# Optimization experiments

Hardware: AMD Instinct MI355X
Metric: run time of the kernel (lower is better)

## Reference

```python
import jax, jax.numpy as jnp
import numpy as np

N_NODES = 100000
N_EDGES = 1600000
IN_SIZE = 512
HID_SIZE = 256
OUT_SIZE = 40
K_STEPS = 10
ALPHA = 0.1


def setup_inputs() -> dict:
    key = jax.random.key(0)
    ks = jax.random.split(key, 8)
    features = jax.random.normal(ks[0], (N_NODES, IN_SIZE), dtype=jnp.float32)
    src = jax.random.randint(ks[1], (N_EDGES,), 0, N_NODES, dtype=jnp.int64)
    dst = jax.random.randint(ks[2], (N_EDGES,), 0, N_NODES, dtype=jnp.int64)
    # MLP params (Kaiming-ish scale)
    W1 = jax.random.normal(ks[3], (IN_SIZE, HID_SIZE), dtype=jnp.float32) / np.sqrt(IN_SIZE)
    b1 = jnp.zeros((HID_SIZE,), dtype=jnp.float32)
    W2 = jax.random.normal(ks[4], (HID_SIZE, OUT_SIZE), dtype=jnp.float32) / np.sqrt(HID_SIZE)
    b2 = jnp.zeros((OUT_SIZE,), dtype=jnp.float32)
    return {"features": features, "src": src, "dst": dst,
            "W1": W1, "b1": b1, "W2": W2, "b2": b2}


def reference(features, src, dst, W1, b1, W2, b2):
    # --- MLP encoder (dropout is identity in eval mode) ---
    h = jax.nn.relu(features @ W1 + b1)
    h = h @ W2 + b2  # [N, out_size]

    # --- Symmetric normalization (DGL APPNPConv, edge_weight=None) ---
    ones_e = jnp.ones((src.shape[0],), dtype=h.dtype)
    deg_out = jax.ops.segment_sum(ones_e, src, num_segments=N_NODES)
    deg_in = jax.ops.segment_sum(ones_e, dst, num_segments=N_NODES)
    norm_src = jnp.power(jnp.clip(deg_out, 1.0), -0.5)[:, None]  # D_out^{-1/2}
    norm_dst = jnp.power(jnp.clip(deg_in, 1.0), -0.5)[:, None]   # D_in^{-1/2}

    # --- k=10 APPNP propagation: h <- (1-a) * D^{-1/2} A D^{-1/2} h + a * h0 ---
    h0 = h

    def step(h, _):
        msg = (h * norm_src)[src]                                  # gather [E, out]
        agg = jax.ops.segment_sum(msg, dst, num_segments=N_NODES)  # scatter-add
        h = (1.0 - ALPHA) * (agg * norm_dst) + ALPHA * h0
        return h, None

    h, _ = jax.lax.scan(step, h, None, length=K_STEPS)
    return h
```

## Files before the change

### kernel.cpp

```cpp
#include <hip/hip_runtime.h>

#define N_NODES 100000
#define N_EDGES 1600000
#define IN_SIZE 512
#define HID_SIZE 256
#define OUT_SIZE 40
#define K_STEPS 10
#define ALPHA 0.1f

#define NCH 250
#define CH_E 6400
#define NBUK 391
#define NRS 8
#define HRS 12544
#define NCS 16
#define CS_E 100000

typedef _Float16 half8 __attribute__((ext_vector_type(8)));
typedef float f32x4 __attribute__((ext_vector_type(4)));

struct __align__(8) Entry { int s; int d; };

__global__ __launch_bounds__(512) void hist_pass(const int* __restrict__ dst,
                                                 int* __restrict__ cnt) {
    __shared__ int h[NBUK];
    const int t = threadIdx.x, c = blockIdx.x;
    for (int j = t; j < NBUK; j += 512) h[j] = 0;
    __syncthreads();
    const int4* d4 = (const int4*)(dst + c * CH_E);
    for (int i = t; i < CH_E / 4; i += 512) {
        const int4 v = d4[i];
        atomicAdd(&h[v.x >> 8], 1);
        atomicAdd(&h[v.y >> 8], 1);
        atomicAdd(&h[v.z >> 8], 1);
        atomicAdd(&h[v.w >> 8], 1);
    }
    __syncthreads();
    for (int j = t; j < NBUK; j += 512) cnt[c * NBUK + j] = h[j];
}

__global__ __launch_bounds__(512) void bucket_scan(const int* __restrict__ cnt,
                                                   int* __restrict__ off,
                                                   int* __restrict__ boff) {
    __shared__ int tot[512];
    const int b = threadIdx.x;
    int s = 0;
    if (b < NBUK)
        for (int c = 0; c < NCH; ++c) s += cnt[c * NBUK + b];
    tot[b] = s;
    __syncthreads();
    for (int o = 1; o < 512; o <<= 1) {
        const int v = (b >= o) ? tot[b - o] : 0;
        __syncthreads();
        tot[b] += v;
        __syncthreads();
    }
    if (b < NBUK) {
        int run = tot[b] - s;
        boff[b] = run;
        for (int c = 0; c < NCH; ++c) { off[c * NBUK + b] = run; run += cnt[c * NBUK + b]; }
        if (b == NBUK - 1) boff[NBUK] = tot[b];
    }
}

__global__ __launch_bounds__(512) void scatter_pass(const int* __restrict__ src,
                                                    const int* __restrict__ dst,
                                                    const int* __restrict__ off,
                                                    Entry* __restrict__ ebuf) {
    __shared__ int cur[NBUK];
    const int t = threadIdx.x, c = blockIdx.x;
    for (int j = t; j < NBUK; j += 512) cur[j] = off[c * NBUK + j];
    __syncthreads();
    const int4* s4 = (const int4*)(src + c * CH_E);
    const int4* d4 = (const int4*)(dst + c * CH_E);
    for (int i = t; i < CH_E / 4; i += 512) {
        const int4 sv = s4[i];
        const int4 dv = d4[i];
        Entry e;
        int p;
        p = atomicAdd(&cur[dv.x >> 8], 1); e.s = sv.x; e.d = dv.x; ebuf[p] = e;
        p = atomicAdd(&cur[dv.y >> 8], 1); e.s = sv.y; e.d = dv.y; ebuf[p] = e;
        p = atomicAdd(&cur[dv.z >> 8], 1); e.s = sv.z; e.d = dv.z; ebuf[p] = e;
        p = atomicAdd(&cur[dv.w >> 8], 1); e.s = sv.w; e.d = dv.w; ebuf[p] = e;
    }
}

__global__ __launch_bounds__(256) void bucket_csr(const Entry* __restrict__ ebuf,
                                                  const int* __restrict__ boff,
                                                  int* __restrict__ rowp,
                                                  float* __restrict__ ndst,
                                                  int* __restrict__ csr) {
    __shared__ int hist[256];
    __shared__ int pref[256];
    __shared__ int cur[256];
    const int t = threadIdx.x, b = blockIdx.x;
    const int beg = boff[b], end = boff[b + 1];
    hist[t] = 0;
    __syncthreads();
    for (int i = beg + t; i < end; i += 256)
        atomicAdd(&hist[ebuf[i].d & 255], 1);
    __syncthreads();
    const int h = hist[t];
    pref[t] = h;
    __syncthreads();
    for (int o = 1; o < 256; o <<= 1) {
        const int v = (t >= o) ? pref[t - o] : 0;
        __syncthreads();
        pref[t] += v;
        __syncthreads();
    }
    const int val = beg + pref[t] - h;
    const int n = (b << 8) + t;
    if (n <= N_NODES) rowp[n] = val;
    if (n < N_NODES) ndst[n] = 1.0f / sqrtf((float)max(h, 1));
    cur[t] = val;
    __syncthreads();
    for (int i = beg + t; i < end; i += 256) {
        const Entry e = ebuf[i];
        const int pos = atomicAdd(&cur[e.d & 255], 1);
        csr[pos] = e.s;
    }
}

__global__ __launch_bounds__(512) void degsrc_part(const int* __restrict__ src,
                                                   int* __restrict__ partial) {
    __shared__ int h[HRS];
    const int t = threadIdx.x;
    const int r = blockIdx.x & (NRS - 1);
    const int c = blockIdx.x >> 3;
    const int base = r * HRS;
    for (int j = t; j < HRS; j += 512) h[j] = 0;
    __syncthreads();
    const int4* s4 = (const int4*)(src + (size_t)c * CS_E);
    for (int i = t; i < CS_E / 4; i += 512) {
        const int4 v = s4[i];
        unsigned u;
        u = (unsigned)(v.x - base); if (u < HRS) atomicAdd(&h[u], 1);
        u = (unsigned)(v.y - base); if (u < HRS) atomicAdd(&h[u], 1);
        u = (unsigned)(v.z - base); if (u < HRS) atomicAdd(&h[u], 1);
        u = (unsigned)(v.w - base); if (u < HRS) atomicAdd(&h[u], 1);
    }
    __syncthreads();
    for (int j = t; j < HRS; j += 512) partial[(size_t)c * (NRS * HRS) + base + j] = h[j];
}

__global__ __launch_bounds__(256) void nsrc_reduce(const int* __restrict__ partial,
                                                   float* __restrict__ nsrc) {
    const int n = blockIdx.x * 256 + threadIdx.x;
    int s = 0;
#pragma unroll
    for (int c = 0; c < NCS; ++c) s += partial[(size_t)c * (NRS * HRS) + n];
    if (n < N_NODES) nsrc[n] = 1.0f / sqrtf((float)max(s, 1));
}

__global__ __launch_bounds__(256) void prep_w1t(const float* __restrict__ W1,
                                                unsigned short* __restrict__ w1t) {
    int idx = blockIdx.x * 256 + threadIdx.x;
    if (idx < IN_SIZE * HID_SIZE) {
        int n = idx >> 9;
        int k = idx & 511;
        _Float16 h = (_Float16)W1[(size_t)k * HID_SIZE + n];
        w1t[idx] = *(unsigned short*)&h;
    }
}

__global__ __launch_bounds__(512) void gemm1_f16(const float* __restrict__ X,
                                                 const unsigned short* __restrict__ w1t,
                                                 const float* __restrict__ b1,
                                                 _Float16* __restrict__ h1) {
    __shared__ __align__(16) _Float16 sA[128 * 64];
    __shared__ __align__(16) _Float16 sB[256 * 64];

    const int t    = threadIdx.x;
    const int lane = t & 63;
    const int w    = t >> 6;
    const int wr   = w >> 2;
    const int wc   = w & 3;
    const int n0   = blockIdx.x * 128;

    f32x4 acc[4][4];
#pragma unroll
    for (int i = 0; i < 4; ++i)
#pragma unroll
        for (int j = 0; j < 4; ++j) acc[i][j] = (f32x4)0.f;

    const int lo = lane & 15;
    const int hi = lane >> 4;
    const int l7 = lane & 7;

    for (int kk = 0; kk < IN_SIZE; kk += 64) {
        __syncthreads();
#pragma unroll
        for (int i = 0; i < 2; ++i) {
            int id  = t + i * 512;
            int row = id >> 3;
            int ch  = id & 7;
            int gr  = n0 + row;
            float4 x0 = make_float4(0.f, 0.f, 0.f, 0.f), x1 = x0;
            if (gr < N_NODES) {
                const float* p = X + (size_t)gr * IN_SIZE + kk + ch * 8;
                x0 = ((const float4*)p)[0];
                x1 = ((const float4*)p)[1];
            }
            half8 hv;
            hv[0] = (_Float16)x0.x; hv[1] = (_Float16)x0.y;
            hv[2] = (_Float16)x0.z; hv[3] = (_Float16)x0.w;
            hv[4] = (_Float16)x1.x; hv[5] = (_Float16)x1.y;
            hv[6] = (_Float16)x1.z; hv[7] = (_Float16)x1.w;
            *(half8*)&sA[row * 64 + ((ch ^ (row & 7)) << 3)] = hv;
        }
#pragma unroll
        for (int i = 0; i < 4; ++i) {
            int id = t + i * 512;
            int n  = id >> 3;
            int ch = id & 7;
            uint4 v = *(const uint4*)(w1t + (size_t)n * IN_SIZE + kk + ch * 8);
            *(uint4*)&sB[n * 64 + ((ch ^ (n & 7)) << 3)] = v;
        }
        __syncthreads();
#pragma unroll
        for (int s = 0; s < 2; ++s) {
            const int chs = ((s * 4 + hi) ^ l7) << 3;
            half8 af[4], bf[4];
#pragma unroll
            for (int f = 0; f < 4; ++f)
                af[f] = *(const half8*)&sA[(wr * 64 + f * 16 + lo) * 64 + chs];
#pragma unroll
            for (int f = 0; f < 4; ++f)
                bf[f] = *(const half8*)&sB[(wc * 64 + f * 16 + lo) * 64 + chs];
#pragma unroll
            for (int fi = 0; fi < 4; ++fi)
#pragma unroll
                for (int fj = 0; fj < 4; ++fj)
                    acc[fi][fj] = __builtin_amdgcn_mfma_f32_16x16x32_f16(
                        af[fi], bf[fj], acc[fi][fj], 0, 0, 0);
        }
    }

    float b1v[4];
#pragma unroll
    for (int fj = 0; fj < 4; ++fj) b1v[fj] = b1[wc * 64 + fj * 16 + lo];
#pragma unroll
    for (int fi = 0; fi < 4; ++fi) {
#pragma unroll
        for (int fj = 0; fj < 4; ++fj) {
            const int col = wc * 64 + fj * 16 + lo;
#pragma unroll
            for (int r = 0; r < 4; ++r) {
                int grow = n0 + wr * 64 + fi * 16 + hi * 4 + r;
                if (grow < N_NODES) {
                    float v = acc[fi][fj][r] + b1v[fj];
                    v = fmaxf(v, 0.f);
                    h1[(size_t)grow * HID_SIZE + col] = (_Float16)v;
                }
            }
        }
    }
}

__global__ __launch_bounds__(256) void gemm2(const _Float16* __restrict__ h1,
                                             const float* __restrict__ W2,
                                             const float* __restrict__ b2,
                                             float* __restrict__ h0) {
    __shared__ __align__(16) float sW2t[40 * 260];
    __shared__ __align__(16) unsigned short sH[64 * 264];

    const int t  = threadIdx.x;
    const int n0 = blockIdx.x * 64;

    for (int idx = t; idx < HID_SIZE * OUT_SIZE; idx += 256) {
        int c = idx / OUT_SIZE;
        int o = idx - c * OUT_SIZE;
        sW2t[o * 260 + c] = W2[idx];
    }
#pragma unroll
    for (int i = 0; i < 8; ++i) {
        int id  = t + i * 256;
        int row = id >> 5;
        int ch  = id & 31;
        uint4 v = make_uint4(0, 0, 0, 0);
        if (n0 + row < N_NODES)
            v = *(const uint4*)(h1 + (size_t)(n0 + row) * HID_SIZE + ch * 8);
        *(uint4*)&sH[row * 264 + ch * 8] = v;
    }
    __syncthreads();

    const int r2 = t >> 2;
    const int q  = t & 3;
    const int o0 = q * 10;
    float acc2[10];
#pragma unroll
    for (int m = 0; m < 10; ++m) acc2[m] = b2[o0 + m];

    for (int c = 0; c < HID_SIZE; c += 8) {
        uint4 hv = *(const uint4*)&sH[r2 * 264 + c];
        const _Float16* hp = (const _Float16*)&hv;
        float f[8];
#pragma unroll
        for (int j = 0; j < 8; ++j) f[j] = (float)hp[j];
#pragma unroll
        for (int m = 0; m < 10; ++m) {
            const float4 w0 = *(const float4*)&sW2t[(o0 + m) * 260 + c];
            const float4 w1 = *(const float4*)&sW2t[(o0 + m) * 260 + c + 4];
            acc2[m] += f[0] * w0.x + f[1] * w0.y + f[2] * w0.z + f[3] * w0.w
                     + f[4] * w1.x + f[5] * w1.y + f[6] * w1.z + f[7] * w1.w;
        }
    }
    if (n0 + r2 < N_NODES) {
        float* dstp = h0 + (size_t)(n0 + r2) * OUT_SIZE + o0;
#pragma unroll
        for (int m = 0; m < 10; ++m) dstp[m] = acc2[m];
    }
}

__global__ __launch_bounds__(320) void g0_init(const float* __restrict__ h0,
                                               const float* __restrict__ nsrc,
                                               _Float16* __restrict__ g) {
    const int tid = threadIdx.x;
    const int ln  = tid / 5;
    const int q   = tid - ln * 5;
    const int n   = blockIdx.x * 64 + ln;
    if (n >= N_NODES) return;
    const float ns = nsrc[n];
    const f32x4 a = *(const f32x4*)(h0 + (size_t)n * OUT_SIZE + q * 8);
    const f32x4 b = *(const f32x4*)(h0 + (size_t)n * OUT_SIZE + q * 8 + 4);
    half8 gv;
    gv[0] = (_Float16)(ns * a[0]); gv[1] = (_Float16)(ns * a[1]);
    gv[2] = (_Float16)(ns * a[2]); gv[3] = (_Float16)(ns * a[3]);
    gv[4] = (_Float16)(ns * b[0]); gv[5] = (_Float16)(ns * b[1]);
    gv[6] = (_Float16)(ns * b[2]); gv[7] = (_Float16)(ns * b[3]);
    *(half8*)(g + (size_t)n * 64 + q * 8) = gv;
}

__global__ __launch_bounds__(320) void appnp_step3(const _Float16* __restrict__ gin,
                                                   const float* __restrict__ h0,
                                                   const int* __restrict__ rowp,
                                                   const int* __restrict__ csr,
                                                   const float* __restrict__ nsrc,
                                                   const float* __restrict__ ndst,
                                                   _Float16* __restrict__ gout,
                                                   float* __restrict__ hout,
                                                   int last) {
    const int tid = threadIdx.x;
    const int ln  = tid / 5;
    const int q   = tid - ln * 5;
    const int n   = blockIdx.x * 64 + ln;
    if (n >= N_NODES) return;

    const int beg = rowp[n];
    const int end = rowp[n + 1];
    const _Float16* gq = gin + q * 8;

    float acc[8];
#pragma unroll
    for (int j = 0; j < 8; ++j) acc[j] = 0.f;

    int e = beg;
    for (; e + 4 <= end; e += 4) {
        const int s0 = csr[e + 0];
        const int s1 = csr[e + 1];
        const int s2 = csr[e + 2];
        const int s3 = csr[e + 3];
        const half8 v0 = *(const half8*)(gq + (size_t)s0 * 64);
        const half8 v1 = *(const half8*)(gq + (size_t)s1 * 64);
        const half8 v2 = *(const half8*)(gq + (size_t)s2 * 64);
        const half8 v3 = *(const half8*)(gq + (size_t)s3 * 64);
#pragma unroll
        for (int j = 0; j < 8; ++j)
            acc[j] += (float)v0[j] + (float)v1[j] + (float)v2[j] + (float)v3[j];
    }
    for (; e < end; ++e) {
        const int s0 = csr[e];
        const half8 v0 = *(const half8*)(gq + (size_t)s0 * 64);
#pragma unroll
        for (int j = 0; j < 8; ++j) acc[j] += (float)v0[j];
    }

    const float nd = (1.0f - ALPHA) * ndst[n];
    const f32x4 h0a = *(const f32x4*)(h0 + (size_t)n * OUT_SIZE + q * 8);
    const f32x4 h0b = *(const f32x4*)(h0 + (size_t)n * OUT_SIZE + q * 8 + 4);
    float r[8];
    r[0] = nd * acc[0] + ALPHA * h0a[0]; r[1] = nd * acc[1] + ALPHA * h0a[1];
    r[2] = nd * acc[2] + ALPHA * h0a[2]; r[3] = nd * acc[3] + ALPHA * h0a[3];
    r[4] = nd * acc[4] + ALPHA * h0b[0]; r[5] = nd * acc[5] + ALPHA * h0b[1];
    r[6] = nd * acc[6] + ALPHA * h0b[2]; r[7] = nd * acc[7] + ALPHA * h0b[3];

    if (last) {
        f32x4 ra, rb;
        ra[0] = r[0]; ra[1] = r[1]; ra[2] = r[2]; ra[3] = r[3];
        rb[0] = r[4]; rb[1] = r[5]; rb[2] = r[6]; rb[3] = r[7];
        *(f32x4*)(hout + (size_t)n * OUT_SIZE + q * 8) = ra;
        *(f32x4*)(hout + (size_t)n * OUT_SIZE + q * 8 + 4) = rb;
    } else {
        const float ns = nsrc[n];
        half8 gv;
#pragma unroll
        for (int j = 0; j < 8; ++j) gv[j] = (_Float16)(ns * r[j]);
        *(half8*)(gout + (size_t)n * 64 + q * 8) = gv;
    }
}

extern "C" void kernel_launch(void* const* d_in, const int* in_sizes, int n_in,
                              void* d_out, int out_size, void* d_ws, size_t ws_size,
                              hipStream_t stream) {
    const float* X   = (const float*)d_in[0];
    const int*   src = (const int*)d_in[1];
    const int*   dst = (const int*)d_in[2];
    const float* W1  = (const float*)d_in[3];
    const float* b1  = (const float*)d_in[4];
    const float* W2  = (const float*)d_in[5];
    const float* b2  = (const float*)d_in[6];
    float* out = (float*)d_out;

    char* ws = (char*)d_ws;
    size_t off = 0;
    auto alloc = [&](size_t bytes) -> void* {
        void* p = ws + off;
        off = (off + bytes + 255) & ~(size_t)255;
        return p;
    };
    float* h0 = (float*)alloc((size_t)N_NODES * OUT_SIZE * 4);
    const size_t mark = off;

    unsigned short* w1t = (unsigned short*)alloc((size_t)IN_SIZE * HID_SIZE * 2);
    _Float16*       h1  = (_Float16*)alloc((size_t)N_NODES * HID_SIZE * 2);

    off = mark;
    _Float16* gA = (_Float16*)alloc((size_t)N_NODES * 64 * 2);
    _Float16* gB = (_Float16*)alloc((size_t)N_NODES * 64 * 2);
    int*   partial = (int*)gA;
    Entry* ebuf    = (Entry*)gB;
    float* nsrc = (float*)alloc((size_t)N_NODES * 4);
    float* ndst = (float*)alloc((size_t)N_NODES * 4);
    int* rowp   = (int*)alloc((size_t)(N_NODES + 2) * 4);
    int* csr    = (int*)alloc((size_t)N_EDGES * 4);
    int* cnt    = (int*)alloc((size_t)NCH * NBUK * 4);
    int* offb   = (int*)alloc((size_t)NCH * NBUK * 4);
    int* boff   = (int*)alloc((size_t)(NBUK + 1) * 4);

    const int pgrid = (N_NODES + 63) / 64;

    prep_w1t<<<(IN_SIZE * HID_SIZE + 255) / 256, 256, 0, stream>>>(W1, w1t);
    gemm1_f16<<<(N_NODES + 127) / 128, 512, 0, stream>>>(X, w1t, b1, h1);
    gemm2<<<(N_NODES + 63) / 64, 256, 0, stream>>>(h1, W2, b2, h0);

    hist_pass<<<NCH, 512, 0, stream>>>(dst, cnt);
    bucket_scan<<<1, 512, 0, stream>>>(cnt, offb, boff);
    scatter_pass<<<NCH, 512, 0, stream>>>(src, dst, offb, ebuf);
    bucket_csr<<<NBUK, 256, 0, stream>>>(ebuf, boff, rowp, ndst, csr);

    degsrc_part<<<NRS * NCS, 512, 0, stream>>>(src, partial);
    nsrc_reduce<<<(NRS * HRS) / 256, 256, 0, stream>>>(partial, nsrc);

    g0_init<<<pgrid, 320, 0, stream>>>(h0, nsrc, gA);

    const _Float16* gin = gA;
    for (int s = 0; s < K_STEPS; ++s) {
        const int last = (s == K_STEPS - 1) ? 1 : 0;
        _Float16* gout = (s & 1) ? gA : gB;
        appnp_step3<<<pgrid, 320, 0, stream>>>(gin, h0, rowp, csr, nsrc, ndst,
                                               gout, out, last);
        gin = gout;
    }
}
```

Baseline: 550.2 us.

## Fuse MLP layers and g0 init into one MFMA kernel with fp16 h0

Merges the first GEMM, the second GEMM (now on MFMA with a padded fp16 W2^T) and the g0 initialisation into a single kernel. The hidden activations stay in LDS instead of making a round trip through a global h1 buffer. The GEMM1 main loop also register-prefetches the next K-slice of X and W1 so loads overlap compute. The residual term is stored once as fp16 ALPHA*h0 in 64-wide rows, which removes the fp32 h0 reads in every propagation step at some cost in precision.

```diff
diff --git a/kernel.cpp b/kernel.cpp
--- a/kernel.cpp
+++ b/kernel.cpp
@@ -153,23 +153,39 @@
     if (n < N_NODES) nsrc[n] = 1.0f / sqrtf((float)max(s, 1));
 }
 
-__global__ __launch_bounds__(256) void prep_w1t(const float* __restrict__ W1,
-                                                unsigned short* __restrict__ w1t) {
+__global__ __launch_bounds__(256) void prep_w(const float* __restrict__ W1,
+                                              const float* __restrict__ W2,
+                                              unsigned short* __restrict__ w1t,
+                                              unsigned short* __restrict__ w2t) {
     int idx = blockIdx.x * 256 + threadIdx.x;
     if (idx < IN_SIZE * HID_SIZE) {
         int n = idx >> 9;
         int k = idx & 511;
         _Float16 h = (_Float16)W1[(size_t)k * HID_SIZE + n];
         w1t[idx] = *(unsigned short*)&h;
-    }
-}
-
-__global__ __launch_bounds__(512) void gemm1_f16(const float* __restrict__ X,
-                                                 const unsigned short* __restrict__ w1t,
-                                                 const float* __restrict__ b1,
-                                                 _Float16* __restrict__ h1) {
-    __shared__ __align__(16) _Float16 sA[128 * 64];
-    __shared__ __align__(16) _Float16 sB[256 * 64];
+    } else if (idx < IN_SIZE * HID_SIZE + 48 * HID_SIZE) {
+        int i2 = idx - IN_SIZE * HID_SIZE;
+        int o = i2 >> 8;
+        int c = i2 & 255;
+        float v = (o < OUT_SIZE) ? W2[(size_t)c * OUT_SIZE + o] : 0.f;
+        _Float16 h = (_Float16)v;
+        w2t[i2] = *(unsigned short*)&h;
+    }
+}
+
+__global__ __launch_bounds__(512) void gemm_fused(const float* __restrict__ X,
+                                                  const unsigned short* __restrict__ w1t,
+                                                  const float* __restrict__ b1,
+                                                  const unsigned short* __restrict__ w2t,
+                                                  const float* __restrict__ b2,
+                                                  const float* __restrict__ nsrc,
+                                                  _Float16* __restrict__ h0a,
+                                                  _Float16* __restrict__ g0) {
+    __shared__ __align__(16) unsigned char lds[49152];
+    _Float16* sA = (_Float16*)lds;
+    _Float16* sB = sA + 128 * 64;
+    _Float16* sC = (_Float16*)lds;
+    _Float16* sW = sC + 128 * 72;
 
     const int t    = threadIdx.x;
     const int lane = t & 63;
@@ -188,34 +204,61 @@
     const int hi = lane >> 4;
     const int l7 = lane & 7;
 
+    int rowA[2], offA[2]; bool okA[2]; const float* pA[2];
+#pragma unroll
+    for (int i = 0; i < 2; ++i) {
+        const int id  = t + i * 512;
+        const int row = id >> 3;
+        const int ch  = id & 7;
+        rowA[i] = row;
+        offA[i] = row * 64 + ((ch ^ (row & 7)) << 3);
+        const int gr = n0 + row;
+        okA[i] = (gr < N_NODES);
+        pA[i] = X + (size_t)(okA[i] ? gr : 0) * IN_SIZE + ch * 8;
+    }
+    int offB[4]; const unsigned short* pB[4];
+#pragma unroll
+    for (int i = 0; i < 4; ++i) {
+        const int id = t + i * 512;
+        const int n  = id >> 3;
+        const int ch = id & 7;
+        offB[i] = n * 64 + ((ch ^ (n & 7)) << 3);
+        pB[i] = w1t + (size_t)n * IN_SIZE + ch * 8;
+    }
+
+    float4 xr[2][2];
+#pragma unroll
+    for (int i = 0; i < 2; ++i) { xr[i][0] = make_float4(0,0,0,0); xr[i][1] = xr[i][0]; }
+    uint4 br[4];
+
+#pragma unroll
+    for (int i = 0; i < 2; ++i)
+        if (okA[i]) { xr[i][0] = ((const float4*)pA[i])[0]; xr[i][1] = ((const float4*)pA[i])[1]; }
+#pragma unroll
+    for (int i = 0; i < 4; ++i) br[i] = *(const uint4*)pB[i];
+
     for (int kk = 0; kk < IN_SIZE; kk += 64) {
         __syncthreads();
 #pragma unroll
         for (int i = 0; i < 2; ++i) {
-            int id  = t + i * 512;
-            int row = id >> 3;
-            int ch  = id & 7;
-            int gr  = n0 + row;
-            float4 x0 = make_float4(0.f, 0.f, 0.f, 0.f), x1 = x0;
-            if (gr < N_NODES) {
-                const float* p = X + (size_t)gr * IN_SIZE + kk + ch * 8;
-                x0 = ((const float4*)p)[0];
-                x1 = ((const float4*)p)[1];
-            }
             half8 hv;
-            hv[0] = (_Float16)x0.x; hv[1] = (_Float16)x0.y;
-            hv[2] = (_Float16)x0.z; hv[3] = (_Float16)x0.w;
-            hv[4] = (_Float16)x1.x; hv[5] = (_Float16)x1.y;
-            hv[6] = (_Float16)x1.z; hv[7] = (_Float16)x1.w;
-            *(half8*)&sA[row * 64 + ((ch ^ (row & 7)) << 3)] = hv;
-        }
-#pragma unroll
-        for (int i = 0; i < 4; ++i) {
-            int id = t + i * 512;
-            int n  = id >> 3;
-            int ch = id & 7;
-            uint4 v = *(const uint4*)(w1t + (size_t)n * IN_SIZE + kk + ch * 8);
-            *(uint4*)&sB[n * 64 + ((ch ^ (n & 7)) << 3)] = v;
+            hv[0] = (_Float16)xr[i][0].x; hv[1] = (_Float16)xr[i][0].y;
+            hv[2] = (_Float16)xr[i][0].z; hv[3] = (_Float16)xr[i][0].w;
+            hv[4] = (_Float16)xr[i][1].x; hv[5] = (_Float16)xr[i][1].y;
+            hv[6] = (_Float16)xr[i][1].z; hv[7] = (_Float16)xr[i][1].w;
+            *(half8*)&sA[offA[i]] = hv;
+        }
+#pragma unroll
+        for (int i = 0; i < 4; ++i) *(uint4*)&sB[offB[i]] = br[i];
+        if (kk + 64 < IN_SIZE) {
+#pragma unroll
+            for (int i = 0; i < 2; ++i)
+                if (okA[i]) {
+                    xr[i][0] = ((const float4*)(pA[i] + kk + 64))[0];
+                    xr[i][1] = ((const float4*)(pA[i] + kk + 64))[1];
+                }
+#pragma unroll
+            for (int i = 0; i < 4; ++i) br[i] = *(const uint4*)(pB[i] + kk + 64);
         }
         __syncthreads();
 #pragma unroll
@@ -240,100 +283,72 @@
     float b1v[4];
 #pragma unroll
     for (int fj = 0; fj < 4; ++fj) b1v[fj] = b1[wc * 64 + fj * 16 + lo];
-#pragma unroll
-    for (int fi = 0; fi < 4; ++fi) {
-#pragma unroll
-        for (int fj = 0; fj < 4; ++fj) {
-            const int col = wc * 64 + fj * 16 + lo;
-#pragma unroll
-            for (int r = 0; r < 4; ++r) {
-                int grow = n0 + wr * 64 + fi * 16 + hi * 4 + r;
-                if (grow < N_NODES) {
-                    float v = acc[fi][fj][r] + b1v[fj];
-                    v = fmaxf(v, 0.f);
-                    h1[(size_t)grow * HID_SIZE + col] = (_Float16)v;
-                }
+
+    __syncthreads();
+#pragma unroll
+    for (int i = 0; i < 3; ++i) {
+        const int id = t + i * 512;
+        const int o  = id >> 5;
+        const int ch = id & 31;
+        const uint4 v = *(const uint4*)(w2t + (size_t)o * HID_SIZE + ch * 8);
+        *(uint4*)&sW[o * 264 + ch * 8] = v;
+    }
+
+    f32x4 acc2[3];
+#pragma unroll
+    for (int f = 0; f < 3; ++f) acc2[f] = (f32x4)0.f;
+    float b2v[3];
+#pragma unroll
+    for (int f = 0; f < 3; ++f) {
+        const int o = f * 16 + lo;
+        b2v[f] = (o < OUT_SIZE) ? b2[o] : 0.f;
+    }
+
+    for (int j = 0; j < 4; ++j) {
+        if (j) __syncthreads();
+        if (wc == j) {
+#pragma unroll
+            for (int fi = 0; fi < 4; ++fi)
+#pragma unroll
+                for (int fj = 0; fj < 4; ++fj)
+#pragma unroll
+                    for (int r = 0; r < 4; ++r) {
+                        const int rl = wr * 64 + fi * 16 + hi * 4 + r;
+                        const int cl = fj * 16 + lo;
+                        const float v = fmaxf(acc[fi][fj][r] + b1v[fj], 0.f);
+                        sC[rl * 72 + cl] = (_Float16)v;
+                    }
+        }
+        __syncthreads();
+#pragma unroll
+        for (int ks = 0; ks < 2; ++ks) {
+            const half8 a = *(const half8*)&sC[(w * 16 + lo) * 72 + ks * 32 + hi * 8];
+#pragma unroll
+            for (int f = 0; f < 3; ++f) {
+                const half8 b = *(const half8*)&sW[(f * 16 + lo) * 264 + j * 64 + ks * 32 + hi * 8];
+                acc2[f] = __builtin_amdgcn_mfma_f32_16x16x32_f16(a, b, acc2[f], 0, 0, 0);
             }
         }
     }
-}
-
-__global__ __launch_bounds__(256) void gemm2(const _Float16* __restrict__ h1,
-                                             const float* __restrict__ W2,
-                                             const float* __restrict__ b2,
-                                             float* __restrict__ h0) {
-    __shared__ __align__(16) float sW2t[40 * 260];
-    __shared__ __align__(16) unsigned short sH[64 * 264];
-
-    const int t  = threadIdx.x;
-    const int n0 = blockIdx.x * 64;
-
-    for (int idx = t; idx < HID_SIZE * OUT_SIZE; idx += 256) {
-        int c = idx / OUT_SIZE;
-        int o = idx - c * OUT_SIZE;
-        sW2t[o * 260 + c] = W2[idx];
-    }
-#pragma unroll
-    for (int i = 0; i < 8; ++i) {
-        int id  = t + i * 256;
-        int row = id >> 5;
-        int ch  = id & 31;
-        uint4 v = make_uint4(0, 0, 0, 0);
-        if (n0 + row < N_NODES)
-            v = *(const uint4*)(h1 + (size_t)(n0 + row) * HID_SIZE + ch * 8);
-        *(uint4*)&sH[row * 264 + ch * 8] = v;
-    }
-    __syncthreads();
-
-    const int r2 = t >> 2;
-    const int q  = t & 3;
-    const int o0 = q * 10;
-    float acc2[10];
-#pragma unroll
-    for (int m = 0; m < 10; ++m) acc2[m] = b2[o0 + m];
-
-    for (int c = 0; c < HID_SIZE; c += 8) {
-        uint4 hv = *(const uint4*)&sH[r2 * 264 + c];
-        const _Float16* hp = (const _Float16*)&hv;
-        float f[8];
-#pragma unroll
-        for (int j = 0; j < 8; ++j) f[j] = (float)hp[j];
-#pragma unroll
-        for (int m = 0; m < 10; ++m) {
-            const float4 w0 = *(const float4*)&sW2t[(o0 + m) * 260 + c];
-            const float4 w1 = *(const float4*)&sW2t[(o0 + m) * 260 + c + 4];
-            acc2[m] += f[0] * w0.x + f[1] * w0.y + f[2] * w0.z + f[3] * w0.w
-                     + f[4] * w1.x + f[5] * w1.y + f[6] * w1.z + f[7] * w1.w;
-        }
-    }
-    if (n0 + r2 < N_NODES) {
-        float* dstp = h0 + (size_t)(n0 + r2) * OUT_SIZE + o0;
-#pragma unroll
-        for (int m = 0; m < 10; ++m) dstp[m] = acc2[m];
-    }
-}
-
-__global__ __launch_bounds__(320) void g0_init(const float* __restrict__ h0,
-                                               const float* __restrict__ nsrc,
-                                               _Float16* __restrict__ g) {
-    const int tid = threadIdx.x;
-    const int ln  = tid / 5;
-    const int q   = tid - ln * 5;
-    const int n   = blockIdx.x * 64 + ln;
-    if (n >= N_NODES) return;
-    const float ns = nsrc[n];
-    const f32x4 a = *(const f32x4*)(h0 + (size_t)n * OUT_SIZE + q * 8);
-    const f32x4 b = *(const f32x4*)(h0 + (size_t)n * OUT_SIZE + q * 8 + 4);
-    half8 gv;
-    gv[0] = (_Float16)(ns * a[0]); gv[1] = (_Float16)(ns * a[1]);
-    gv[2] = (_Float16)(ns * a[2]); gv[3] = (_Float16)(ns * a[3]);
-    gv[4] = (_Float16)(ns * b[0]); gv[5] = (_Float16)(ns * b[1]);
-    gv[6] = (_Float16)(ns * b[2]); gv[7] = (_Float16)(ns * b[3]);
-    *(half8*)(g + (size_t)n * 64 + q * 8) = gv;
-}
-
-__global__ __launch_bounds__(320) void appnp_step3(const _Float16* __restrict__ gin,
-                                                   const float* __restrict__ h0,
+
+#pragma unroll
+    for (int f = 0; f < 3; ++f) {
+        const int o = f * 16 + lo;
+#pragma unroll
+        for (int r = 0; r < 4; ++r) {
+            const int grow = n0 + w * 16 + hi * 4 + r;
+            if (grow < N_NODES && o < OUT_SIZE) {
+                const float v = acc2[f][r] + b2v[f];
+                const float ns = nsrc[grow];
+                g0 [(size_t)grow * 64 + o] = (_Float16)(ns * v);
+                h0a[(size_t)grow * 64 + o] = (_Float16)(ALPHA * v);
+            }
+        }
+    }
+}
+
+__global__ __launch_bounds__(320) void appnp_step4(const _Float16* __restrict__ gin,
+                                                   const _Float16* __restrict__ h0a,
                                                    const int* __restrict__ rowp,
                                                    const int* __restrict__ csr,
                                                    const float* __restrict__ nsrc,
@@ -377,13 +392,10 @@
     }
 
     const float nd = (1.0f - ALPHA) * ndst[n];
-    const f32x4 h0a = *(const f32x4*)(h0 + (size_t)n * OUT_SIZE + q * 8);
-    const f32x4 h0b = *(const f32x4*)(h0 + (size_t)n * OUT_SIZE + q * 8 + 4);
+    const half8 ha = *(const half8*)(h0a + (size_t)n * 64 + q * 8);
     float r[8];
-    r[0] = nd * acc[0] + ALPHA * h0a[0]; r[1] = nd * acc[1] + ALPHA * h0a[1];
-    r[2] = nd * acc[2] + ALPHA * h0a[2]; r[3] = nd * acc[3] + ALPHA * h0a[3];
-    r[4] = nd * acc[4] + ALPHA * h0b[0]; r[5] = nd * acc[5] + ALPHA * h0b[1];
-    r[6] = nd * acc[6] + ALPHA * h0b[2]; r[7] = nd * acc[7] + ALPHA * h0b[3];
+#pragma unroll
+    for (int j = 0; j < 8; ++j) r[j] = nd * acc[j] + (float)ha[j];
 
     if (last) {
         f32x4 ra, rb;
@@ -419,17 +431,11 @@
         off = (off + bytes + 255) & ~(size_t)255;
         return p;
     };
-    float* h0 = (float*)alloc((size_t)N_NODES * OUT_SIZE * 4);
-    const size_t mark = off;
-
-    unsigned short* w1t = (unsigned short*)alloc((size_t)IN_SIZE * HID_SIZE * 2);
-    _Float16*       h1  = (_Float16*)alloc((size_t)N_NODES * HID_SIZE * 2);
-
-    off = mark;
-    _Float16* gA = (_Float16*)alloc((size_t)N_NODES * 64 * 2);
-    _Float16* gB = (_Float16*)alloc((size_t)N_NODES * 64 * 2);
-    int*   partial = (int*)gA;
-    Entry* ebuf    = (Entry*)gB;
+    _Float16* h0a = (_Float16*)alloc((size_t)N_NODES * 64 * 2);
+    _Float16* gA  = (_Float16*)alloc((size_t)N_NODES * 64 * 2);
+    _Float16* gB  = (_Float16*)alloc((size_t)N_NODES * 64 * 2);
+    Entry* ebuf    = (Entry*)gA;
+    int*   partial = (int*)gB;
     float* nsrc = (float*)alloc((size_t)N_NODES * 4);
     float* ndst = (float*)alloc((size_t)N_NODES * 4);
     int* rowp   = (int*)alloc((size_t)(N_NODES + 2) * 4);
@@ -437,28 +443,26 @@
     int* cnt    = (int*)alloc((size_t)NCH * NBUK * 4);
     int* offb   = (int*)alloc((size_t)NCH * NBUK * 4);
     int* boff   = (int*)alloc((size_t)(NBUK + 1) * 4);
+    unsigned short* w1t = (unsigned short*)alloc((size_t)IN_SIZE * HID_SIZE * 2);
+    unsigned short* w2t = (unsigned short*)alloc((size_t)48 * HID_SIZE * 2);
 
     const int pgrid = (N_NODES + 63) / 64;
-
-    prep_w1t<<<(IN_SIZE * HID_SIZE + 255) / 256, 256, 0, stream>>>(W1, w1t);
-    gemm1_f16<<<(N_NODES + 127) / 128, 512, 0, stream>>>(X, w1t, b1, h1);
-    gemm2<<<(N_NODES + 63) / 64, 256, 0, stream>>>(h1, W2, b2, h0);
 
     hist_pass<<<NCH, 512, 0, stream>>>(dst, cnt);
     bucket_scan<<<1, 512, 0, stream>>>(cnt, offb, boff);
     scatter_pass<<<NCH, 512, 0, stream>>>(src, dst, offb, ebuf);
     bucket_csr<<<NBUK, 256, 0, stream>>>(ebuf, boff, rowp, ndst, csr);
-
     degsrc_part<<<NRS * NCS, 512, 0, stream>>>(src, partial);
     nsrc_reduce<<<(NRS * HRS) / 256, 256, 0, stream>>>(partial, nsrc);
 
-    g0_init<<<pgrid, 320, 0, stream>>>(h0, nsrc, gA);
+    prep_w<<<(IN_SIZE * HID_SIZE + 48 * HID_SIZE + 255) / 256, 256, 0, stream>>>(W1, W2, w1t, w2t);
+    gemm_fused<<<(N_NODES + 127) / 128, 512, 0, stream>>>(X, w1t, b1, w2t, b2, nsrc, h0a, gA);
 
     const _Float16* gin = gA;
     for (int s = 0; s < K_STEPS; ++s) {
         const int last = (s == K_STEPS - 1) ? 1 : 0;
         _Float16* gout = (s & 1) ? gA : gB;
-        appnp_step3<<<pgrid, 320, 0, stream>>>(gin, h0, rowp, csr, nsrc, ndst,
+        appnp_step4<<<pgrid, 320, 0, stream>>>(gin, h0a, rowp, csr, nsrc, ndst,
                                                gout, out, last);
         gin = gout;
     }
```

Measured after the change: 548.9 us. About the same (-0.2%).
